# Optimization experiments

Hardware: AMD Instinct MI355X
Metric: run time of the kernel (lower is better)

Reference implementation:

```python
import jax, jax.numpy as jnp
import numpy as np

N = 50000
E_RAND = 800000
IN_CH = 128
HID = 128
HEADS = 8
HEAD_DIM = HID // HEADS  # 16
NUM_CLASSES = 40
NEG_SLOPE = 0.2


def _gatv2_conv(x, src, dst, Wl, Wr, att, b, concat):
    # Wl, Wr: [F_in, H*C]; att: [H, C]; b: [H*C] or [C]
    H, C = att.shape
    xl = (x @ Wl).reshape(N, H, C)  # source-side projection
    xr = (x @ Wr).reshape(N, H, C)  # target-side projection
    e = jax.nn.leaky_relu(xl[src] + xr[dst], NEG_SLOPE)      # [E,H,C]
    logits = jnp.einsum('ehc,hc->eh', e, att)                # [E,H]
    lmax = jax.ops.segment_max(logits, dst, num_segments=N)  # [N,H]
    lmax = jnp.where(jnp.isfinite(lmax), lmax, 0.0)
    p = jnp.exp(logits - lmax[dst])                          # [E,H]
    denom = jax.ops.segment_sum(p, dst, num_segments=N)      # [N,H]
    alpha = p / jnp.maximum(denom[dst], 1e-16)               # segment softmax
    out = jax.ops.segment_sum(xl[src] * alpha[:, :, None], dst, num_segments=N)  # [N,H,C]
    out = out.reshape(N, H * C) if concat else out.mean(axis=1)
    return out + b


def setup_inputs() -> dict:
    key = jax.random.key(0)
    ks = jax.random.split(key, 16)
    x = jax.random.normal(ks[0], (N, IN_CH), dtype=jnp.float32)
    src = jax.random.randint(ks[1], (E_RAND,), 0, N)
    dst = jax.random.randint(ks[2], (E_RAND,), 0, N)
    loops = jnp.arange(N)  # PyG GATv2Conv adds self-loops by default
    edge_src = jnp.concatenate([src, loops]).astype(jnp.int64)
    edge_dst = jnp.concatenate([dst, loops]).astype(jnp.int64)

    def glorot(k, shape):
        fan = shape[0] + shape[1]
        s = jnp.sqrt(6.0 / fan)
        return jax.random.uniform(k, shape, jnp.float32, -s, s)

    # layer 0: 128 -> 8 heads x 16, concat
    Wl0 = glorot(ks[3], (IN_CH, HID)); Wr0 = glorot(ks[4], (IN_CH, HID))
    att0 = glorot(ks[5], (HEADS, HEAD_DIM)); b0 = jnp.zeros((HID,), jnp.float32)
    # layer 1: 128 -> 8 heads x 16, concat
    Wl1 = glorot(ks[6], (HID, HID)); Wr1 = glorot(ks[7], (HID, HID))
    att1 = glorot(ks[8], (HEADS, HEAD_DIM)); b1 = jnp.zeros((HID,), jnp.float32)
    # layer 2: 128 -> 1 head x 40, no concat (mean == identity for 1 head)
    Wl2 = glorot(ks[9], (HID, NUM_CLASSES)); Wr2 = glorot(ks[10], (HID, NUM_CLASSES))
    att2 = glorot(ks[11], (1, NUM_CLASSES)); b2 = jnp.zeros((NUM_CLASSES,), jnp.float32)

    return {"x": x, "edge_src": edge_src, "edge_dst": edge_dst,
            "Wl0": Wl0, "Wr0": Wr0, "att0": att0, "b0": b0,
            "Wl1": Wl1, "Wr1": Wr1, "att1": att1, "b1": b1,
            "Wl2": Wl2, "Wr2": Wr2, "att2": att2, "b2": b2}


def reference(x, edge_src, edge_dst, Wl0, Wr0, att0, b0, Wl1, Wr1, att1, b1,
              Wl2, Wr2, att2, b2):
    # Inference mode: F.dropout(training=False) is identity.
    h = _gatv2_conv(x, edge_src, edge_dst, Wl0, Wr0, att0, b0, concat=True)
    h = jax.nn.relu(h)
    h = _gatv2_conv(h, edge_src, edge_dst, Wl1, Wr1, att1, b1, concat=True)
    h = jax.nn.relu(h)
    out = _gatv2_conv(h, edge_src, edge_dst, Wl2, Wr2, att2, b2, concat=False)
    return out
```

## Files before the change

### kernel.cpp

```cpp
#include <hip/hip_runtime.h>
#include <hip/hip_fp16.h>
#include <cmath>

typedef _Float16 half8 __attribute__((ext_vector_type(8)));
typedef _Float16 h2 __attribute__((ext_vector_type(2)));
typedef float f32x4 __attribute__((ext_vector_type(4)));

#define BINCAP 2600
#define BSTRIDE (BINCAP + 384)
#define NBINS_MAX 512

__device__ __forceinline__ float dpp_add_xor1(float t) {
    int r = __builtin_amdgcn_update_dpp(0, __float_as_int(t), 0xB1, 0xF, 0xF, true);
    return t + __int_as_float(r);
}
__device__ __forceinline__ float dpp_add_xor2(float t) {
    int r = __builtin_amdgcn_update_dpp(0, __float_as_int(t), 0x4E, 0xF, 0xF, true);
    return t + __int_as_float(r);
}

__device__ __forceinline__ float hdot2(h2 a, h2 b, float acc) {
#if __has_builtin(__builtin_amdgcn_fdot2)
    return __builtin_amdgcn_fdot2(a, b, acc, false);
#else
    return acc + (float)a[0] * (float)b[0] + (float)a[1] * (float)b[1];
#endif
}

__global__ __launch_bounds__(256) void bin_edges(const int* __restrict__ src,
                                                 const int* __restrict__ dst,
                                                 int* __restrict__ binCnt,
                                                 unsigned* __restrict__ binned,
                                                 int E, int nbins)
{
    __shared__ int hist[NBINS_MAX];
    __shared__ int ofs[NBINS_MAX];
    int tid = threadIdx.x;
    for (int i = tid; i < nbins; i += 256) hist[i] = 0;
    __syncthreads();
    int chunk = (E + gridDim.x - 1) / gridDim.x;
    int e0 = blockIdx.x * chunk;
    int e1 = min(e0 + chunk, E);
    for (int e = e0 + tid; e < e1; e += 256)
        atomicAdd(&hist[dst[e] >> 7], 1);
    __syncthreads();
    for (int b = tid; b < nbins; b += 256) {
        int h = hist[b];
        ofs[b] = (h > 0) ? atomicAdd(&binCnt[b], h) : 0;
    }
    __syncthreads();
    for (int e = e0 + tid; e < e1; e += 256) {
        int d = dst[e];
        int b = d >> 7;
        int p = atomicAdd(&ofs[b], 1);
        if (p < BINCAP)
            binned[(size_t)b * BINCAP + p] = (unsigned)src[e] | ((unsigned)(d & 127) << 16);
    }
}

__global__ __launch_bounds__(256) void bin_to_csr(const int* __restrict__ binCnt,
                                                  const unsigned* __restrict__ binned,
                                                  int* __restrict__ bucket,
                                                  int2* __restrict__ meta, int N)
{
    __shared__ int dcnt[128], ps[128], dpos[128];
    __shared__ int sbuf[BSTRIDE];
    __shared__ int tot_s;
    int b = blockIdx.x, tid = threadIdx.x;
    int nb = min(binCnt[b], BINCAP);
    size_t inbase = (size_t)b * BINCAP;
    size_t outbase = (size_t)b * BSTRIDE;
    if (tid < 128) dcnt[tid] = 0;
    __syncthreads();
    for (int i = tid; i < nb; i += 256)
        atomicAdd(&dcnt[(binned[inbase + i] >> 16) & 127], 1);
    __syncthreads();
    int pc = 0;
    if (tid < 128) { pc = (dcnt[tid] + 3) & ~3; ps[tid] = pc; }
    __syncthreads();
    for (int o = 1; o < 128; o <<= 1) {
        int v = (tid < 128 && tid >= o) ? ps[tid - o] : 0;
        __syncthreads();
        if (tid < 128) ps[tid] += v;
        __syncthreads();
    }
    if (tid < 128) {
        int dofs = ps[tid] - pc;
        dpos[tid] = dofs;
        for (int k = dcnt[tid]; k < pc; ++k) sbuf[dofs + k] = 0;
        int gd = b * 128 + tid;
        if (gd < N) meta[gd] = make_int2((int)outbase + dofs, dcnt[tid]);
        if (tid == 127) tot_s = ps[127];
    }
    __syncthreads();
    for (int i = tid; i < nb; i += 256) {
        unsigned u = binned[inbase + i];
        int p = atomicAdd(&dpos[(u >> 16) & 127], 1);
        sbuf[p] = (int)(u & 0xFFFFu);
    }
    __syncthreads();
    int tot = min(tot_s, BSTRIDE);
    for (int i = tid; i < tot; i += 256)
        bucket[outbase + i] = sbuf[i];
}

__global__ void wt_build(const float* __restrict__ Wl0, const float* __restrict__ Wr0,
                         const float* __restrict__ Wl1, const float* __restrict__ Wr1,
                         const float* __restrict__ Wl2, const float* __restrict__ Wr2,
                         __half* __restrict__ Wt0, __half* __restrict__ Wt1,
                         __half* __restrict__ Wt2) {
    int i = blockIdx.x * blockDim.x + threadIdx.x;
    const int T01 = 256 * 128, T2 = 80 * 128;
    if (i < T01) {
        int c = i >> 7, k = i & 127;
        float v = (c < 128) ? Wl0[k * 128 + c] : Wr0[k * 128 + (c - 128)];
        Wt0[i] = __float2half(v);
    } else if (i < 2 * T01) {
        int j = i - T01;
        int c = j >> 7, k = j & 127;
        float v = (c < 128) ? Wl1[k * 128 + c] : Wr1[k * 128 + (c - 128)];
        Wt1[j] = __float2half(v);
    } else if (i < 2 * T01 + T2) {
        int j = i - 2 * T01;
        int c = j >> 7, k = j & 127;
        float v = (c < 40) ? Wl2[k * 40 + c] : Wr2[k * 40 + (c - 40)];
        Wt2[j] = __float2half(v);
    }
}

template<int OUTH, bool HIN>
__global__ __launch_bounds__(256) void proj_mfma(const void* __restrict__ xin,
                                                 const __half* __restrict__ Wt,
                                                 __half* __restrict__ xl,
                                                 __half* __restrict__ xr,
                                                 int n)
{
    constexpr int OUTT = 2 * OUTH;
    constexpr int CT = OUTT / 16;
    __shared__ uint4 lds[1024 + OUTT * 16];
    int t = threadIdx.x;
    int r0 = blockIdx.x * 64;
    {
        int row = t >> 2;
        int k0 = (t & 3) * 32;
        int gr = r0 + row;
        #pragma unroll
        for (int s = 0; s < 4; ++s) {
            union { uint4 u; _Float16 h[8]; } pk;
            if (gr < n) {
                if constexpr (HIN) {
                    const uint4* xp = (const uint4*)((const __half*)xin + (size_t)gr * 128 + k0);
                    pk.u = xp[s];
                } else {
                    const float4* xp = (const float4*)((const float*)xin + (size_t)gr * 128 + k0 + s * 8);
                    float4 f0 = xp[0], f1 = xp[1];
                    pk.h[0] = (_Float16)f0.x; pk.h[1] = (_Float16)f0.y;
                    pk.h[2] = (_Float16)f0.z; pk.h[3] = (_Float16)f0.w;
                    pk.h[4] = (_Float16)f1.x; pk.h[5] = (_Float16)f1.y;
                    pk.h[6] = (_Float16)f1.z; pk.h[7] = (_Float16)f1.w;
                }
            } else {
                pk.u = make_uint4(0, 0, 0, 0);
            }
            int j = (t & 3) * 4 + s;
            lds[row * 16 + (j ^ (row & 7))] = pk.u;
        }
    }
    {
        const uint4* Wtv = (const uint4*)Wt;
        for (int m = t; m < OUTT * 16; m += 256) {
            int c = m >> 4, j = m & 15;
            lds[1024 + c * 16 + (j ^ (c & 7))] = Wtv[m];
        }
    }
    __syncthreads();
    int w = t >> 6, l = t & 63;
    int lr = l & 15, lg = l >> 4;
    half8 af[4];
    {
        int row = w * 16 + lr;
        #pragma unroll
        for (int kb = 0; kb < 4; ++kb) {
            int j = kb * 4 + lg;
            af[kb] = *reinterpret_cast<const half8*>(&lds[row * 16 + (j ^ (row & 7))]);
        }
    }
    f32x4 acc[CT];
    #pragma unroll
    for (int ct = 0; ct < CT; ++ct) acc[ct] = (f32x4){0.f, 0.f, 0.f, 0.f};
    int csw = lr & 7;
    #pragma unroll
    for (int ct = 0; ct < CT; ++ct) {
        int c = ct * 16 + lr;
        #pragma unroll
        for (int kb = 0; kb < 4; ++kb) {
            int j = kb * 4 + lg;
            half8 bf = *reinterpret_cast<const half8*>(&lds[1024 + c * 16 + (j ^ csw)]);
            acc[ct] = __builtin_amdgcn_mfma_f32_16x16x32_f16(af[kb], bf, acc[ct], 0, 0, 0);
        }
    }
    #pragma unroll
    for (int ct = 0; ct < CT; ++ct) {
        int c = ct * 16 + lr;
        #pragma unroll
        for (int i = 0; i < 4; ++i) {
            int gr = r0 + w * 16 + lg * 4 + i;
            if (gr < n) {
                __half h = __float2half(acc[ct][i]);
                if (c < OUTH) xl[(size_t)gr * OUTH + c] = h;
                else          xr[(size_t)gr * OUTH + (c - OUTH)] = h;
            }
        }
    }
}

__global__ void aggr128(const int2* __restrict__ meta, const int* __restrict__ bucket,
                        const __half* __restrict__ xlh, const __half* __restrict__ xrh,
                        const float* __restrict__ att, const float* __restrict__ bias,
                        __half* __restrict__ outp, int N, int do_relu)
{
    int wave = threadIdx.x >> 6;
    int lane = threadIdx.x & 63;
    int grp = lane >> 4;
    int j = lane & 15;
    int nd = (blockIdx.x * (blockDim.x >> 6) + wave) * 4 + grp;
    if (nd >= N) return;
    union { uint4 u; h2 h[4]; } rq;
    rq.u = ((const uint4*)xrh)[(size_t)nd * 16 + j];
    h2 a2[4];
    {
        float4 t0 = ((const float4*)att)[2 * j];
        float4 t1 = ((const float4*)att)[2 * j + 1];
        a2[0] = h2{(_Float16)t0.x, (_Float16)t0.y};
        a2[1] = h2{(_Float16)t0.z, (_Float16)t0.w};
        a2[2] = h2{(_Float16)t1.x, (_Float16)t1.y};
        a2[3] = h2{(_Float16)t1.z, (_Float16)t1.w};
    }
    const uint4* xlv = (const uint4*)xlh;
    int2 md = meta[nd];
    int beg = md.x, deg = md.y;
    const int* brow = bucket + beg;
    const h2 c02 = h2{(_Float16)0.2f, (_Float16)0.2f};
    float s0 = 0.f, s1 = 0.f, s2 = 0.f, s3 = 0.f;
    float o0[8], o1[8], o2[8], o3[8];
    #pragma unroll
    for (int i = 0; i < 8; ++i) { o0[i] = 0.f; o1[i] = 0.f; o2[i] = 0.f; o3[i] = 0.f; }
    for (int p = 0; p < deg; p += 4) {
        int4 ss = *(const int4*)(brow + p);
        union { uint4 u; h2 h[4]; } q0, q1, q2, q3;
        q0.u = xlv[(size_t)ss.x * 16 + j];
        q1.u = xlv[(size_t)ss.y * 16 + j];
        q2.u = xlv[(size_t)ss.z * 16 + j];
        q3.u = xlv[(size_t)ss.w * 16 + j];
        {
            float t = 0.f;
            #pragma unroll
            for (int i = 0; i < 4; ++i) {
                h2 v2 = q0.h[i] + rq.h[i];
                h2 lk = __builtin_elementwise_max(v2, v2 * c02);
                t = hdot2(lk, a2[i], t);
            }
            t = dpp_add_xor1(t);
            float pe = __expf(t);
            s0 += pe;
            #pragma unroll
            for (int i = 0; i < 4; ++i) {
                o0[2*i]   = fmaf(pe, (float)q0.h[i][0], o0[2*i]);
                o0[2*i+1] = fmaf(pe, (float)q0.h[i][1], o0[2*i+1]);
            }
        }
        {
            float t = 0.f;
            #pragma unroll
            for (int i = 0; i < 4; ++i) {
                h2 v2 = q1.h[i] + rq.h[i];
                h2 lk = __builtin_elementwise_max(v2, v2 * c02);
                t = hdot2(lk, a2[i], t);
            }
            t = dpp_add_xor1(t);
            float pe = (p + 1 < deg) ? __expf(t) : 0.f;
            s1 += pe;
            #pragma unroll
            for (int i = 0; i < 4; ++i) {
                o1[2*i]   = fmaf(pe, (float)q1.h[i][0], o1[2*i]);
                o1[2*i+1] = fmaf(pe, (float)q1.h[i][1], o1[2*i+1]);
            }
        }
        {
            float t = 0.f;
            #pragma unroll
            for (int i = 0; i < 4; ++i) {
                h2 v2 = q2.h[i] + rq.h[i];
                h2 lk = __builtin_elementwise_max(v2, v2 * c02);
                t = hdot2(lk, a2[i], t);
            }
            t = dpp_add_xor1(t);
            float pe = (p + 2 < deg) ? __expf(t) : 0.f;
            s2 += pe;
            #pragma unroll
            for (int i = 0; i < 4; ++i) {
                o2[2*i]   = fmaf(pe, (float)q2.h[i][0], o2[2*i]);
                o2[2*i+1] = fmaf(pe, (float)q2.h[i][1], o2[2*i+1]);
            }
        }
        {
            float t = 0.f;
            #pragma unroll
            for (int i = 0; i < 4; ++i) {
                h2 v2 = q3.h[i] + rq.h[i];
                h2 lk = __builtin_elementwise_max(v2, v2 * c02);
                t = hdot2(lk, a2[i], t);
            }
            t = dpp_add_xor1(t);
            float pe = (p + 3 < deg) ? __expf(t) : 0.f;
            s3 += pe;
            #pragma unroll
            for (int i = 0; i < 4; ++i) {
                o3[2*i]   = fmaf(pe, (float)q3.h[i][0], o3[2*i]);
                o3[2*i+1] = fmaf(pe, (float)q3.h[i][1], o3[2*i+1]);
            }
        }
    }
    float s = (s0 + s1) + (s2 + s3);
    {
        float inv = 1.f / fmaxf(s, 1e-16f);
        float4 b0 = ((const float4*)bias)[2 * j];
        float4 b1 = ((const float4*)bias)[2 * j + 1];
        float w[8];
        #pragma unroll
        for (int i = 0; i < 8; ++i)
            w[i] = ((o0[i] + o1[i]) + (o2[i] + o3[i])) * inv;
        w[0] += b0.x; w[1] += b0.y; w[2] += b0.z; w[3] += b0.w;
        w[4] += b1.x; w[5] += b1.y; w[6] += b1.z; w[7] += b1.w;
        if (do_relu) {
            #pragma unroll
            for (int i = 0; i < 8; ++i) w[i] = fmaxf(w[i], 0.f);
        }
        union { uint4 u; __half2 h[4]; } ow;
        ow.h[0] = __floats2half2_rn(w[0], w[1]);
        ow.h[1] = __floats2half2_rn(w[2], w[3]);
        ow.h[2] = __floats2half2_rn(w[4], w[5]);
        ow.h[3] = __floats2half2_rn(w[6], w[7]);
        ((uint4*)outp)[(size_t)nd * 16 + j] = ow.u;
    }
}

__global__ void aggr40(const int2* __restrict__ meta, const int* __restrict__ bucket,
                       const __half* __restrict__ xlh, const __half* __restrict__ xrh,
                       const float* __restrict__ att, const float* __restrict__ bias,
                       float* __restrict__ outp, int N)
{
    int wave = threadIdx.x >> 6;
    int lane = threadIdx.x & 63;
    int grp = lane >> 4;
    int j = lane & 15;
    int nd = (blockIdx.x * (blockDim.x >> 6) + wave) * 4 + grp;
    if (nd >= N) return;
    bool act = (j < 10);
    union { uint2 u; h2 h[2]; } rq;
    rq.u = make_uint2(0, 0);
    h2 a2[2] = {h2{(_Float16)0.f, (_Float16)0.f}, h2{(_Float16)0.f, (_Float16)0.f}};
    if (act) {
        rq.u = *(const uint2*)(xrh + (size_t)nd * 40 + 4 * j);
        float4 a4 = ((const float4*)att)[j];
        a2[0] = h2{(_Float16)a4.x, (_Float16)a4.y};
        a2[1] = h2{(_Float16)a4.z, (_Float16)a4.w};
    }
    int2 md = meta[nd];
    int beg = md.x, deg = md.y;
    const int* brow = bucket + beg;
    const h2 c02 = h2{(_Float16)0.2f, (_Float16)0.2f};
    float s0 = 0.f, s1 = 0.f;
    float o0[4], o1[4];
    #pragma unroll
    for (int i = 0; i < 4; ++i) { o0[i] = 0.f; o1[i] = 0.f; }
    for (int p = 0; p < deg; p += 4) {
        int4 ss = *(const int4*)(brow + p);
        union { uint2 u; h2 h[2]; } q0, q1, q2, q3;
        q0.u = act ? *(const uint2*)(xlh + (size_t)ss.x * 40 + 4 * j) : make_uint2(0, 0);
        q1.u = act ? *(const uint2*)(xlh + (size_t)ss.y * 40 + 4 * j) : make_uint2(0, 0);
        q2.u = act ? *(const uint2*)(xlh + (size_t)ss.z * 40 + 4 * j) : make_uint2(0, 0);
        q3.u = act ? *(const uint2*)(xlh + (size_t)ss.w * 40 + 4 * j) : make_uint2(0, 0);
        {
            float t = 0.f;
            #pragma unroll
            for (int i = 0; i < 2; ++i) {
                h2 v2 = q0.h[i] + rq.h[i];
                h2 lk = __builtin_elementwise_max(v2, v2 * c02);
                t = hdot2(lk, a2[i], t);
            }
            t = dpp_add_xor1(t); t = dpp_add_xor2(t);
            t += __shfl_xor(t, 4); t += __shfl_xor(t, 8);
            float pe = __expf(t);
            s0 += pe;
            #pragma unroll
            for (int i = 0; i < 2; ++i) {
                o0[2*i]   = fmaf(pe, (float)q0.h[i][0], o0[2*i]);
                o0[2*i+1] = fmaf(pe, (float)q0.h[i][1], o0[2*i+1]);
            }
        }
        {
            float t = 0.f;
            #pragma unroll
            for (int i = 0; i < 2; ++i) {
                h2 v2 = q1.h[i] + rq.h[i];
                h2 lk = __builtin_elementwise_max(v2, v2 * c02);
                t = hdot2(lk, a2[i], t);
            }
            t = dpp_add_xor1(t); t = dpp_add_xor2(t);
            t += __shfl_xor(t, 4); t += __shfl_xor(t, 8);
            float pe = (p + 1 < deg) ? __expf(t) : 0.f;
            s1 += pe;
            #pragma unroll
            for (int i = 0; i < 2; ++i) {
                o1[2*i]   = fmaf(pe, (float)q1.h[i][0], o1[2*i]);
                o1[2*i+1] = fmaf(pe, (float)q1.h[i][1], o1[2*i+1]);
            }
        }
        {
            float t = 0.f;
            #pragma unroll
            for (int i = 0; i < 2; ++i) {
                h2 v2 = q2.h[i] + rq.h[i];
                h2 lk = __builtin_elementwise_max(v2, v2 * c02);
                t = hdot2(lk, a2[i], t);
            }
            t = dpp_add_xor1(t); t = dpp_add_xor2(t);
            t += __shfl_xor(t, 4); t += __shfl_xor(t, 8);
            float pe = (p + 2 < deg) ? __expf(t) : 0.f;
            s0 += pe;
            #pragma unroll
            for (int i = 0; i < 2; ++i) {
                o0[2*i]   = fmaf(pe, (float)q2.h[i][0], o0[2*i]);
                o0[2*i+1] = fmaf(pe, (float)q2.h[i][1], o0[2*i+1]);
            }
        }
        {
            float t = 0.f;
            #pragma unroll
            for (int i = 0; i < 2; ++i) {
                h2 v2 = q3.h[i] + rq.h[i];
                h2 lk = __builtin_elementwise_max(v2, v2 * c02);
                t = hdot2(lk, a2[i], t);
            }
            t = dpp_add_xor1(t); t = dpp_add_xor2(t);
            t += __shfl_xor(t, 4); t += __shfl_xor(t, 8);
            float pe = (p + 3 < deg) ? __expf(t) : 0.f;
            s1 += pe;
            #pragma unroll
            for (int i = 0; i < 2; ++i) {
                o1[2*i]   = fmaf(pe, (float)q3.h[i][0], o1[2*i]);
                o1[2*i+1] = fmaf(pe, (float)q3.h[i][1], o1[2*i+1]);
            }
        }
    }
    if (act) {
        float s = s0 + s1;
        float inv = 1.f / fmaxf(s, 1e-16f);
        float4 b4 = ((const float4*)bias)[j];
        float4 w;
        w.x = (o0[0] + o1[0]) * inv + b4.x;
        w.y = (o0[1] + o1[1]) * inv + b4.y;
        w.z = (o0[2] + o1[2]) * inv + b4.z;
        w.w = (o0[3] + o1[3]) * inv + b4.w;
        *(float4*)(outp + (size_t)nd * 40 + 4 * j) = w;
    }
}

extern "C" void kernel_launch(void* const* d_in, const int* in_sizes, int n_in,
                              void* d_out, int out_size, void* d_ws, size_t ws_size,
                              hipStream_t stream)
{
    const float* x    = (const float*)d_in[0];
    const int*   esrc = (const int*)d_in[1];
    const int*   edst = (const int*)d_in[2];
    const float* Wl0  = (const float*)d_in[3];
    const float* Wr0  = (const float*)d_in[4];
    const float* att0 = (const float*)d_in[5];
    const float* b0   = (const float*)d_in[6];
    const float* Wl1  = (const float*)d_in[7];
    const float* Wr1  = (const float*)d_in[8];
    const float* att1 = (const float*)d_in[9];
    const float* b1   = (const float*)d_in[10];
    const float* Wl2  = (const float*)d_in[11];
    const float* Wr2  = (const float*)d_in[12];
    const float* att2 = (const float*)d_in[13];
    const float* b2   = (const float*)d_in[14];
    float* out = (float*)d_out;

    const int N = in_sizes[0] / 128;
    const int E = in_sizes[1];
    const int nbins = (N + 127) / 128;

    char* ws = (char*)d_ws;
    size_t off = 0;
    auto walloc = [&](size_t bytes) -> void* {
        void* p = ws + off;
        off = (off + bytes + 255) & ~(size_t)255;
        return p;
    };
    __half*   xlh    = (__half*)walloc((size_t)N * 128 * 2);
    __half*   xrh    = (__half*)walloc((size_t)N * 128 * 2);
    __half*   hbuf   = (__half*)walloc((size_t)N * 128 * 2);
    __half*   Wt0    = (__half*)walloc(256 * 128 * 2);
    __half*   Wt1    = (__half*)walloc(256 * 128 * 2);
    __half*   Wt2    = (__half*)walloc(80 * 128 * 2);
    int*      binCnt = (int*)walloc((size_t)nbins * 4);
    unsigned* binned = (unsigned*)walloc((size_t)nbins * BINCAP * 4);
    int*      bucket = (int*)walloc((size_t)nbins * BSTRIDE * 4);
    int2*     meta   = (int2*)walloc((size_t)N * 8);

    wt_build<<<(2 * 256 * 128 + 80 * 128 + 255) / 256, 256, 0, stream>>>(
        Wl0, Wr0, Wl1, Wr1, Wl2, Wr2, Wt0, Wt1, Wt2);

    hipMemsetAsync(binCnt, 0, (size_t)nbins * 4, stream);
    bin_edges<<<256, 256, 0, stream>>>(esrc, edst, binCnt, binned, E, nbins);
    bin_to_csr<<<nbins, 256, 0, stream>>>(binCnt, binned, bucket, meta, N);

    int nblk = (N + 15) / 16;
    int pblk = (N + 63) / 64;

    proj_mfma<128, false><<<pblk, 256, 0, stream>>>(x, Wt0, xlh, xrh, N);
    aggr128<<<nblk, 256, 0, stream>>>(meta, bucket, xlh, xrh, att0, b0, hbuf, N, 1);
    proj_mfma<128, true><<<pblk, 256, 0, stream>>>(hbuf, Wt1, xlh, xrh, N);
    aggr128<<<nblk, 256, 0, stream>>>(meta, bucket, xlh, xrh, att1, b1, hbuf, N, 1);
    proj_mfma<40, true><<<pblk, 256, 0, stream>>>(hbuf, Wt2, xlh, xrh, N);
    aggr40<<<nblk, 256, 0, stream>>>(meta, bucket, xlh, xrh, att2, b2, out, N);
}
```

Baseline: 182.6 us.

## Partition each node's neighbor list by source-index octant and sync blocks per octant

The CSR build now splits each destination's neighbor list into 8 sub-lists by the top bits of the source index, stores per-octant counts in a widened meta record, and pads each sub-list to even length. The aggregation kernels walk octants in order and place a block barrier after each, so all waves in a block gather from the same slice of the feature table at roughly the same time. The aim is better L2 locality for the random gathers. In exchange it adds barriers, extra padding, a more complex binning pass, a larger per-bin stride, and it removes the early exit for out-of-range nodes so they can join the barriers.

```diff
diff --git a/kernel.cpp b/kernel.cpp
--- a/kernel.cpp
+++ b/kernel.cpp
@@ -7,7 +7,7 @@
 typedef float f32x4 __attribute__((ext_vector_type(4)));
 
 #define BINCAP 2600
-#define BSTRIDE (BINCAP + 384)
+#define BSTRIDE 3700
 #define NBINS_MAX 512
 
 __device__ __forceinline__ float dpp_add_xor1(float t) {
@@ -61,22 +61,37 @@
 __global__ __launch_bounds__(256) void bin_to_csr(const int* __restrict__ binCnt,
                                                   const unsigned* __restrict__ binned,
                                                   int* __restrict__ bucket,
-                                                  int2* __restrict__ meta, int N)
+                                                  int4* __restrict__ meta, int N)
 {
-    __shared__ int dcnt[128], ps[128], dpos[128];
+    __shared__ int dq[128 * 8];
+    __shared__ int qof[128 * 8];
+    __shared__ int ps[128];
     __shared__ int sbuf[BSTRIDE];
     __shared__ int tot_s;
     int b = blockIdx.x, tid = threadIdx.x;
     int nb = min(binCnt[b], BINCAP);
     size_t inbase = (size_t)b * BINCAP;
     size_t outbase = (size_t)b * BSTRIDE;
-    if (tid < 128) dcnt[tid] = 0;
-    __syncthreads();
-    for (int i = tid; i < nb; i += 256)
-        atomicAdd(&dcnt[(binned[inbase + i] >> 16) & 127], 1);
-    __syncthreads();
-    int pc = 0;
-    if (tid < 128) { pc = (dcnt[tid] + 3) & ~3; ps[tid] = pc; }
+    for (int i = tid; i < 128 * 8; i += 256) dq[i] = 0;
+    __syncthreads();
+    for (int i = tid; i < nb; i += 256) {
+        unsigned u = binned[inbase + i];
+        int d = (u >> 16) & 127;
+        int oct = (u & 0xFFFFu) >> 13;
+        atomicAdd(&dq[d * 8 + oct], 1);
+    }
+    __syncthreads();
+    int total = 0;
+    if (tid < 128) {
+        int run = 0;
+        #pragma unroll
+        for (int o = 0; o < 8; ++o) {
+            qof[tid * 8 + o] = run;
+            run += (dq[tid * 8 + o] + 1) & ~1;
+        }
+        total = run;
+        ps[tid] = run;
+    }
     __syncthreads();
     for (int o = 1; o < 128; o <<= 1) {
         int v = (tid < 128 && tid >= o) ? ps[tid - o] : 0;
@@ -85,17 +100,34 @@
         __syncthreads();
     }
     if (tid < 128) {
-        int dofs = ps[tid] - pc;
-        dpos[tid] = dofs;
-        for (int k = dcnt[tid]; k < pc; ++k) sbuf[dofs + k] = 0;
+        int dbeg = ps[tid] - total;
+        int deg = 0, p0 = 0, p1 = 0;
+        #pragma unroll
+        for (int o = 0; o < 8; ++o) {
+            int c = dq[tid * 8 + o];
+            deg += c;
+            if (o < 4) p0 |= (c << (8 * o));
+            else       p1 |= (c << (8 * (o - 4)));
+        }
         int gd = b * 128 + tid;
-        if (gd < N) meta[gd] = make_int2((int)outbase + dofs, dcnt[tid]);
+        if (gd < N) meta[gd] = make_int4((int)outbase + dbeg, deg, p0, p1);
+        #pragma unroll
+        for (int o = 0; o < 8; ++o) {
+            int c = dq[tid * 8 + o];
+            int qs = dbeg + qof[tid * 8 + o];
+            if (c & 1) sbuf[qs + c] = 0;
+            qof[tid * 8 + o] = qs;
+        }
         if (tid == 127) tot_s = ps[127];
     }
+    __syncthreads();
+    for (int i = tid; i < 128 * 8; i += 256) dq[i] = 0;
     __syncthreads();
     for (int i = tid; i < nb; i += 256) {
         unsigned u = binned[inbase + i];
-        int p = atomicAdd(&dpos[(u >> 16) & 127], 1);
+        int d = (u >> 16) & 127;
+        int oct = (u & 0xFFFFu) >> 13;
+        int p = qof[d * 8 + oct] + atomicAdd(&dq[d * 8 + oct], 1);
         sbuf[p] = (int)(u & 0xFFFFu);
     }
     __syncthreads();
@@ -214,7 +246,7 @@
     }
 }
 
-__global__ void aggr128(const int2* __restrict__ meta, const int* __restrict__ bucket,
+__global__ void aggr128(const int4* __restrict__ meta, const int* __restrict__ bucket,
                         const __half* __restrict__ xlh, const __half* __restrict__ xrh,
                         const float* __restrict__ att, const float* __restrict__ bias,
                         __half* __restrict__ outp, int N, int do_relu)
@@ -224,9 +256,10 @@
     int grp = lane >> 4;
     int j = lane & 15;
     int nd = (blockIdx.x * (blockDim.x >> 6) + wave) * 4 + grp;
-    if (nd >= N) return;
+    bool valid = nd < N;
+    int ndc = valid ? nd : 0;
     union { uint4 u; h2 h[4]; } rq;
-    rq.u = ((const uint4*)xrh)[(size_t)nd * 16 + j];
+    rq.u = ((const uint4*)xrh)[(size_t)ndc * 16 + j];
     h2 a2[4];
     {
         float4 t0 = ((const float4*)att)[2 * j];
@@ -237,92 +270,100 @@
         a2[3] = h2{(_Float16)t1.z, (_Float16)t1.w};
     }
     const uint4* xlv = (const uint4*)xlh;
-    int2 md = meta[nd];
-    int beg = md.x, deg = md.y;
-    const int* brow = bucket + beg;
+    int4 md = meta[ndc];
+    int qpos = md.x;
+    int p0 = valid ? md.z : 0;
+    int p1 = valid ? md.w : 0;
     const h2 c02 = h2{(_Float16)0.2f, (_Float16)0.2f};
     float s0 = 0.f, s1 = 0.f, s2 = 0.f, s3 = 0.f;
     float o0[8], o1[8], o2[8], o3[8];
     #pragma unroll
     for (int i = 0; i < 8; ++i) { o0[i] = 0.f; o1[i] = 0.f; o2[i] = 0.f; o3[i] = 0.f; }
-    for (int p = 0; p < deg; p += 4) {
-        int4 ss = *(const int4*)(brow + p);
-        union { uint4 u; h2 h[4]; } q0, q1, q2, q3;
-        q0.u = xlv[(size_t)ss.x * 16 + j];
-        q1.u = xlv[(size_t)ss.y * 16 + j];
-        q2.u = xlv[(size_t)ss.z * 16 + j];
-        q3.u = xlv[(size_t)ss.w * 16 + j];
-        {
-            float t = 0.f;
-            #pragma unroll
-            for (int i = 0; i < 4; ++i) {
-                h2 v2 = q0.h[i] + rq.h[i];
-                h2 lk = __builtin_elementwise_max(v2, v2 * c02);
-                t = hdot2(lk, a2[i], t);
-            }
-            t = dpp_add_xor1(t);
-            float pe = __expf(t);
-            s0 += pe;
-            #pragma unroll
-            for (int i = 0; i < 4; ++i) {
-                o0[2*i]   = fmaf(pe, (float)q0.h[i][0], o0[2*i]);
-                o0[2*i+1] = fmaf(pe, (float)q0.h[i][1], o0[2*i+1]);
-            }
-        }
-        {
-            float t = 0.f;
-            #pragma unroll
-            for (int i = 0; i < 4; ++i) {
-                h2 v2 = q1.h[i] + rq.h[i];
-                h2 lk = __builtin_elementwise_max(v2, v2 * c02);
-                t = hdot2(lk, a2[i], t);
-            }
-            t = dpp_add_xor1(t);
-            float pe = (p + 1 < deg) ? __expf(t) : 0.f;
-            s1 += pe;
-            #pragma unroll
-            for (int i = 0; i < 4; ++i) {
-                o1[2*i]   = fmaf(pe, (float)q1.h[i][0], o1[2*i]);
-                o1[2*i+1] = fmaf(pe, (float)q1.h[i][1], o1[2*i+1]);
-            }
-        }
-        {
-            float t = 0.f;
-            #pragma unroll
-            for (int i = 0; i < 4; ++i) {
-                h2 v2 = q2.h[i] + rq.h[i];
-                h2 lk = __builtin_elementwise_max(v2, v2 * c02);
-                t = hdot2(lk, a2[i], t);
-            }
-            t = dpp_add_xor1(t);
-            float pe = (p + 2 < deg) ? __expf(t) : 0.f;
-            s2 += pe;
-            #pragma unroll
-            for (int i = 0; i < 4; ++i) {
-                o2[2*i]   = fmaf(pe, (float)q2.h[i][0], o2[2*i]);
-                o2[2*i+1] = fmaf(pe, (float)q2.h[i][1], o2[2*i+1]);
-            }
-        }
-        {
-            float t = 0.f;
-            #pragma unroll
-            for (int i = 0; i < 4; ++i) {
-                h2 v2 = q3.h[i] + rq.h[i];
-                h2 lk = __builtin_elementwise_max(v2, v2 * c02);
-                t = hdot2(lk, a2[i], t);
-            }
-            t = dpp_add_xor1(t);
-            float pe = (p + 3 < deg) ? __expf(t) : 0.f;
-            s3 += pe;
-            #pragma unroll
-            for (int i = 0; i < 4; ++i) {
-                o3[2*i]   = fmaf(pe, (float)q3.h[i][0], o3[2*i]);
-                o3[2*i+1] = fmaf(pe, (float)q3.h[i][1], o3[2*i+1]);
-            }
-        }
+    for (int oct = 0; oct < 8; ++oct) {
+        int qc = ((oct < 4 ? p0 : p1) >> ((oct & 3) * 8)) & 255;
+        int qpad = (qc + 1) & ~1;
+        for (int p = 0; p < qpad; p += 4) {
+            int2 i01 = *(const int2*)(bucket + qpos + p);
+            int2 i23 = (p + 2 < qpad) ? *(const int2*)(bucket + qpos + p + 2) : i01;
+            union { uint4 u; h2 h[4]; } q0, q1, q2, q3;
+            q0.u = xlv[(size_t)i01.x * 16 + j];
+            q1.u = xlv[(size_t)i01.y * 16 + j];
+            q2.u = xlv[(size_t)i23.x * 16 + j];
+            q3.u = xlv[(size_t)i23.y * 16 + j];
+            {
+                float t = 0.f;
+                #pragma unroll
+                for (int i = 0; i < 4; ++i) {
+                    h2 v2 = q0.h[i] + rq.h[i];
+                    h2 lk = __builtin_elementwise_max(v2, v2 * c02);
+                    t = hdot2(lk, a2[i], t);
+                }
+                t = dpp_add_xor1(t);
+                float pe = (p < qc) ? __expf(t) : 0.f;
+                s0 += pe;
+                #pragma unroll
+                for (int i = 0; i < 4; ++i) {
+                    o0[2*i]   = fmaf(pe, (float)q0.h[i][0], o0[2*i]);
+                    o0[2*i+1] = fmaf(pe, (float)q0.h[i][1], o0[2*i+1]);
+                }
+            }
+            {
+                float t = 0.f;
+                #pragma unroll
+                for (int i = 0; i < 4; ++i) {
+                    h2 v2 = q1.h[i] + rq.h[i];
+                    h2 lk = __builtin_elementwise_max(v2, v2 * c02);
+                    t = hdot2(lk, a2[i], t);
+                }
+                t = dpp_add_xor1(t);
+                float pe = (p + 1 < qc) ? __expf(t) : 0.f;
+                s1 += pe;
+                #pragma unroll
+                for (int i = 0; i < 4; ++i) {
+                    o1[2*i]   = fmaf(pe, (float)q1.h[i][0], o1[2*i]);
+                    o1[2*i+1] = fmaf(pe, (float)q1.h[i][1], o1[2*i+1]);
+                }
+            }
+            {
+                float t = 0.f;
+                #pragma unroll
+                for (int i = 0; i < 4; ++i) {
+                    h2 v2 = q2.h[i] + rq.h[i];
+                    h2 lk = __builtin_elementwise_max(v2, v2 * c02);
+                    t = hdot2(lk, a2[i], t);
+                }
+                t = dpp_add_xor1(t);
+                float pe = (p + 2 < qc) ? __expf(t) : 0.f;
+                s2 += pe;
+                #pragma unroll
+                for (int i = 0; i < 4; ++i) {
+                    o2[2*i]   = fmaf(pe, (float)q2.h[i][0], o2[2*i]);
+                    o2[2*i+1] = fmaf(pe, (float)q2.h[i][1], o2[2*i+1]);
+                }
+            }
+            {
+                float t = 0.f;
+                #pragma unroll
+                for (int i = 0; i < 4; ++i) {
+                    h2 v2 = q3.h[i] + rq.h[i];
+                    h2 lk = __builtin_elementwise_max(v2, v2 * c02);
+                    t = hdot2(lk, a2[i], t);
+                }
+                t = dpp_add_xor1(t);
+                float pe = (p + 3 < qc) ? __expf(t) : 0.f;
+                s3 += pe;
+                #pragma unroll
+                for (int i = 0; i < 4; ++i) {
+                    o3[2*i]   = fmaf(pe, (float)q3.h[i][0], o3[2*i]);
+                    o3[2*i+1] = fmaf(pe, (float)q3.h[i][1], o3[2*i+1]);
+                }
+            }
+        }
+        qpos += qpad;
+        __syncthreads();
     }
     float s = (s0 + s1) + (s2 + s3);
-    {
+    if (valid) {
         float inv = 1.f / fmaxf(s, 1e-16f);
         float4 b0 = ((const float4*)bias)[2 * j];
         float4 b1 = ((const float4*)bias)[2 * j + 1];
@@ -345,7 +386,7 @@
     }
 }
 
-__global__ void aggr40(const int2* __restrict__ meta, const int* __restrict__ bucket,
+__global__ void aggr40(const int4* __restrict__ meta, const int* __restrict__ bucket,
                        const __half* __restrict__ xlh, const __half* __restrict__ xrh,
                        const float* __restrict__ att, const float* __restrict__ bias,
                        float* __restrict__ outp, int N)
@@ -355,106 +396,115 @@
     int grp = lane >> 4;
     int j = lane & 15;
     int nd = (blockIdx.x * (blockDim.x >> 6) + wave) * 4 + grp;
-    if (nd >= N) return;
+    bool valid = nd < N;
+    int ndc = valid ? nd : 0;
     bool act = (j < 10);
     union { uint2 u; h2 h[2]; } rq;
     rq.u = make_uint2(0, 0);
     h2 a2[2] = {h2{(_Float16)0.f, (_Float16)0.f}, h2{(_Float16)0.f, (_Float16)0.f}};
     if (act) {
-        rq.u = *(const uint2*)(xrh + (size_t)nd * 40 + 4 * j);
+        rq.u = *(const uint2*)(xrh + (size_t)ndc * 40 + 4 * j);
         float4 a4 = ((const float4*)att)[j];
         a2[0] = h2{(_Float16)a4.x, (_Float16)a4.y};
         a2[1] = h2{(_Float16)a4.z, (_Float16)a4.w};
     }
-    int2 md = meta[nd];
-    int beg = md.x, deg = md.y;
-    const int* brow = bucket + beg;
+    int4 md = meta[ndc];
+    int qpos = md.x;
+    int p0 = valid ? md.z : 0;
+    int p1 = valid ? md.w : 0;
     const h2 c02 = h2{(_Float16)0.2f, (_Float16)0.2f};
     float s0 = 0.f, s1 = 0.f;
     float o0[4], o1[4];
     #pragma unroll
     for (int i = 0; i < 4; ++i) { o0[i] = 0.f; o1[i] = 0.f; }
-    for (int p = 0; p < deg; p += 4) {
-        int4 ss = *(const int4*)(brow + p);
-        union { uint2 u; h2 h[2]; } q0, q1, q2, q3;
-        q0.u = act ? *(const uint2*)(xlh + (size_t)ss.x * 40 + 4 * j) : make_uint2(0, 0);
-        q1.u = act ? *(const uint2*)(xlh + (size_t)ss.y * 40 + 4 * j) : make_uint2(0, 0);
-        q2.u = act ? *(const uint2*)(xlh + (size_t)ss.z * 40 + 4 * j) : make_uint2(0, 0);
-        q3.u = act ? *(const uint2*)(xlh + (size_t)ss.w * 40 + 4 * j) : make_uint2(0, 0);
-        {
-            float t = 0.f;
-            #pragma unroll
-            for (int i = 0; i < 2; ++i) {
-                h2 v2 = q0.h[i] + rq.h[i];
-                h2 lk = __builtin_elementwise_max(v2, v2 * c02);
-                t = hdot2(lk, a2[i], t);
-            }
-            t = dpp_add_xor1(t); t = dpp_add_xor2(t);
-            t += __shfl_xor(t, 4); t += __shfl_xor(t, 8);
-            float pe = __expf(t);
-            s0 += pe;
-            #pragma unroll
-            for (int i = 0; i < 2; ++i) {
-                o0[2*i]   = fmaf(pe, (float)q0.h[i][0], o0[2*i]);
-                o0[2*i+1] = fmaf(pe, (float)q0.h[i][1], o0[2*i+1]);
-            }
-        }
-        {
-            float t = 0.f;
-            #pragma unroll
-            for (int i = 0; i < 2; ++i) {
-                h2 v2 = q1.h[i] + rq.h[i];
-                h2 lk = __builtin_elementwise_max(v2, v2 * c02);
-                t = hdot2(lk, a2[i], t);
-            }
-            t = dpp_add_xor1(t); t = dpp_add_xor2(t);
-            t += __shfl_xor(t, 4); t += __shfl_xor(t, 8);
-            float pe = (p + 1 < deg) ? __expf(t) : 0.f;
-            s1 += pe;
-            #pragma unroll
-            for (int i = 0; i < 2; ++i) {
-                o1[2*i]   = fmaf(pe, (float)q1.h[i][0], o1[2*i]);
-                o1[2*i+1] = fmaf(pe, (float)q1.h[i][1], o1[2*i+1]);
-            }
-        }
-        {
-            float t = 0.f;
-            #pragma unroll
-            for (int i = 0; i < 2; ++i) {
-                h2 v2 = q2.h[i] + rq.h[i];
-                h2 lk = __builtin_elementwise_max(v2, v2 * c02);
-                t = hdot2(lk, a2[i], t);
-            }
-            t = dpp_add_xor1(t); t = dpp_add_xor2(t);
-            t += __shfl_xor(t, 4); t += __shfl_xor(t, 8);
-            float pe = (p + 2 < deg) ? __expf(t) : 0.f;
-            s0 += pe;
-            #pragma unroll
-            for (int i = 0; i < 2; ++i) {
-                o0[2*i]   = fmaf(pe, (float)q2.h[i][0], o0[2*i]);
-                o0[2*i+1] = fmaf(pe, (float)q2.h[i][1], o0[2*i+1]);
-            }
-        }
-        {
-            float t = 0.f;
-            #pragma unroll
-            for (int i = 0; i < 2; ++i) {
-                h2 v2 = q3.h[i] + rq.h[i];
-                h2 lk = __builtin_elementwise_max(v2, v2 * c02);
-                t = hdot2(lk, a2[i], t);
-            }
-            t = dpp_add_xor1(t); t = dpp_add_xor2(t);
-            t += __shfl_xor(t, 4); t += __shfl_xor(t, 8);
-            float pe = (p + 3 < deg) ? __expf(t) : 0.f;
-            s1 += pe;
-            #pragma unroll
-            for (int i = 0; i < 2; ++i) {
-                o1[2*i]   = fmaf(pe, (float)q3.h[i][0], o1[2*i]);
-                o1[2*i+1] = fmaf(pe, (float)q3.h[i][1], o1[2*i+1]);
-            }
-        }
-    }
-    if (act) {
+    for (int oct = 0; oct < 8; ++oct) {
+        int qc = ((oct < 4 ? p0 : p1) >> ((oct & 3) * 8)) & 255;
+        int qpad = (qc + 1) & ~1;
+        for (int p = 0; p < qpad; p += 4) {
+            int2 i01 = *(const int2*)(bucket + qpos + p);
+            int2 i23 = (p + 2 < qpad) ? *(const int2*)(bucket + qpos + p + 2) : i01;
+            union { uint2 u; h2 h[2]; } q0, q1, q2, q3;
+            q0.u = act ? *(const uint2*)(xlh + (size_t)i01.x * 40 + 4 * j) : make_uint2(0, 0);
+            q1.u = act ? *(const uint2*)(xlh + (size_t)i01.y * 40 + 4 * j) : make_uint2(0, 0);
+            q2.u = act ? *(const uint2*)(xlh + (size_t)i23.x * 40 + 4 * j) : make_uint2(0, 0);
+            q3.u = act ? *(const uint2*)(xlh + (size_t)i23.y * 40 + 4 * j) : make_uint2(0, 0);
+            {
+                float t = 0.f;
+                #pragma unroll
+                for (int i = 0; i < 2; ++i) {
+                    h2 v2 = q0.h[i] + rq.h[i];
+                    h2 lk = __builtin_elementwise_max(v2, v2 * c02);
+                    t = hdot2(lk, a2[i], t);
+                }
+                t = dpp_add_xor1(t); t = dpp_add_xor2(t);
+                t += __shfl_xor(t, 4); t += __shfl_xor(t, 8);
+                float pe = (p < qc) ? __expf(t) : 0.f;
+                s0 += pe;
+                #pragma unroll
+                for (int i = 0; i < 2; ++i) {
+                    o0[2*i]   = fmaf(pe, (float)q0.h[i][0], o0[2*i]);
+                    o0[2*i+1] = fmaf(pe, (float)q0.h[i][1], o0[2*i+1]);
+                }
+            }
+            {
+                float t = 0.f;
+                #pragma unroll
+                for (int i = 0; i < 2; ++i) {
+                    h2 v2 = q1.h[i] + rq.h[i];
+                    h2 lk = __builtin_elementwise_max(v2, v2 * c02);
+                    t = hdot2(lk, a2[i], t);
+                }
+                t = dpp_add_xor1(t); t = dpp_add_xor2(t);
+                t += __shfl_xor(t, 4); t += __shfl_xor(t, 8);
+                float pe = (p + 1 < qc) ? __expf(t) : 0.f;
+                s1 += pe;
+                #pragma unroll
+                for (int i = 0; i < 2; ++i) {
+                    o1[2*i]   = fmaf(pe, (float)q1.h[i][0], o1[2*i]);
+                    o1[2*i+1] = fmaf(pe, (float)q1.h[i][1], o1[2*i+1]);
+                }
+            }
+            {
+                float t = 0.f;
+                #pragma unroll
+                for (int i = 0; i < 2; ++i) {
+                    h2 v2 = q2.h[i] + rq.h[i];
+                    h2 lk = __builtin_elementwise_max(v2, v2 * c02);
+                    t = hdot2(lk, a2[i], t);
+                }
+                t = dpp_add_xor1(t); t = dpp_add_xor2(t);
+                t += __shfl_xor(t, 4); t += __shfl_xor(t, 8);
+                float pe = (p + 2 < qc) ? __expf(t) : 0.f;
+                s0 += pe;
+                #pragma unroll
+                for (int i = 0; i < 2; ++i) {
+                    o0[2*i]   = fmaf(pe, (float)q2.h[i][0], o0[2*i]);
+                    o0[2*i+1] = fmaf(pe, (float)q2.h[i][1], o0[2*i+1]);
+                }
+            }
+            {
+                float t = 0.f;
+                #pragma unroll
+                for (int i = 0; i < 2; ++i) {
+                    h2 v2 = q3.h[i] + rq.h[i];
+                    h2 lk = __builtin_elementwise_max(v2, v2 * c02);
+                    t = hdot2(lk, a2[i], t);
+                }
+                t = dpp_add_xor1(t); t = dpp_add_xor2(t);
+                t += __shfl_xor(t, 4); t += __shfl_xor(t, 8);
+                float pe = (p + 3 < qc) ? __expf(t) : 0.f;
+                s1 += pe;
+                #pragma unroll
+                for (int i = 0; i < 2; ++i) {
+                    o1[2*i]   = fmaf(pe, (float)q3.h[i][0], o1[2*i]);
+                    o1[2*i+1] = fmaf(pe, (float)q3.h[i][1], o1[2*i+1]);
+                }
+            }
+        }
+        qpos += qpad;
+        __syncthreads();
+    }
+    if (valid && act) {
         float s = s0 + s1;
         float inv = 1.f / fmaxf(s, 1e-16f);
         float4 b4 = ((const float4*)bias)[j];
@@ -508,7 +558,7 @@
     int*      binCnt = (int*)walloc((size_t)nbins * 4);
     unsigned* binned = (unsigned*)walloc((size_t)nbins * BINCAP * 4);
     int*      bucket = (int*)walloc((size_t)nbins * BSTRIDE * 4);
-    int2*     meta   = (int2*)walloc((size_t)N * 8);
+    int4*     meta   = (int4*)walloc((size_t)N * 16);
 
     wt_build<<<(2 * 256 * 128 + 80 * 128 + 255) / 256, 256, 0, stream>>>(
         Wl0, Wr0, Wl1, Wr1, Wl2, Wr2, Wt0, Wt1, Wt2);
```

Measured after the change: 252.8 us. 1.38x slower.
